# Performance work log

Hardware: AMD Instinct MI355X
Metric: run time of the kernel (lower is better)

The kernel has to match this reference:

```python
import jax, jax.numpy as jnp
import numpy as np

HEAD_SIZE = 256
HEAD_SIZE_R = HEAD_SIZE // 4   # 64, RoPE slice
HEAD_SIZE_C = HEAD_SIZE - HEAD_SIZE_R  # 192
N_EMBD = 256


def rope(x, start_pos=0):
    # x: [B, T, d_r] with interleaved (even, odd) pairs
    B, T, d = x.shape
    half = d // 2
    theta = 1.0 / (10000.0 ** (jnp.arange(half, dtype=x.dtype) / half))  # [half]
    idx = jnp.arange(start_pos, start_pos + T, dtype=x.dtype)[:, None] * theta[None, :]  # [T, half]
    sin, cos = jnp.sin(idx), jnp.cos(idx)
    xs = x.reshape(B, T, half, 2)
    x1, x2 = xs[..., 0], xs[..., 1]
    rot = jnp.stack([x1 * cos - x2 * sin, x1 * sin + x2 * cos], axis=-1)
    return rot.reshape(B, T, d)


def setup_inputs() -> dict:
    key = jax.random.key(0)
    ks = jax.random.split(key, 8)
    B, T = 32, 2048
    s = 0.05
    return {
        "x": jax.random.normal(ks[0], (B, T, N_EMBD), dtype=jnp.float32),
        "Wq_comp": jax.random.normal(ks[1], (N_EMBD, N_EMBD), dtype=jnp.float32) * s,
        "Wkv_comp": jax.random.normal(ks[2], (N_EMBD, N_EMBD), dtype=jnp.float32) * s,
        "Wqc": jax.random.normal(ks[3], (N_EMBD, HEAD_SIZE_C), dtype=jnp.float32) * s,
        "Wqr": jax.random.normal(ks[4], (N_EMBD, HEAD_SIZE_R), dtype=jnp.float32) * s,
        "Wkc": jax.random.normal(ks[5], (N_EMBD, HEAD_SIZE_C), dtype=jnp.float32) * s,
        "Wkr": jax.random.normal(ks[6], (N_EMBD, HEAD_SIZE_R), dtype=jnp.float32) * s,
        "Wv": jax.random.normal(ks[7], (N_EMBD, HEAD_SIZE), dtype=jnp.float32) * s,
    }


def reference(x, Wq_comp, Wkv_comp, Wqc, Wqr, Wkc, Wkr, Wv):
    # Low-rank compression
    c_q = x @ Wq_comp      # [B,T,C]
    c_kv = x @ Wkv_comp    # [B,T,C]
    # Q: content + rotary slice
    q_c = c_q @ Wqc                      # [B,T,192]
    q_r = rope(c_q @ Wqr, start_pos=0)   # [B,T,64]
    q = jnp.concatenate([q_c, q_r], axis=-1)  # [B,T,256]
    # K: content + rotary slice
    k_c = c_kv @ Wkc
    k_r = rope(c_kv @ Wkr, start_pos=0)
    k = jnp.concatenate([k_c, k_r], axis=-1)  # [B,T,256]
    v = c_kv @ Wv                              # [B,T,256]
    # Causal attention (dropout is identity in eval)
    scale = 1.0 / jnp.sqrt(jnp.asarray(HEAD_SIZE, dtype=x.dtype))
    wei = jnp.einsum('bqd,bkd->bqk', q, k) * scale  # [B,T,T]
    T_q = q.shape[1]
    mask = jnp.tril(jnp.ones((T_q, T_q), dtype=bool))
    wei = jnp.where(mask, wei, jnp.asarray(-jnp.inf, dtype=wei.dtype))
    wei = jax.nn.softmax(wei, axis=-1)
    out = jnp.einsum('bqk,bkd->bqd', wei, v)  # [B,T,256]
    return out, (k, v)
```

## Files before the change

### kernel.cpp

```cpp
#include <hip/hip_runtime.h>

typedef float  f32x4  __attribute__((ext_vector_type(4)));
typedef __bf16 bf16x8 __attribute__((ext_vector_type(8)));
typedef unsigned short u16x8 __attribute__((ext_vector_type(8)));
typedef unsigned short u16x4 __attribute__((ext_vector_type(4)));

#define DEV static __device__ __forceinline__

DEV unsigned short f2b(float f) {
  unsigned int u = __float_as_uint(f);
  u += 0x7fffu + ((u >> 16) & 1u);
  return (unsigned short)(u >> 16);
}
DEV float b2f(unsigned short h) { return __uint_as_float(((unsigned int)h) << 16); }

DEV f32x4 mfma16(bf16x8 a, bf16x8 b, f32x4 c) {
  return __builtin_amdgcn_mfma_f32_16x16x32_bf16(a, b, c, 0, 0, 0);
}

__global__ __launch_bounds__(256) void k_prep(
    const float* __restrict__ Wq_comp, const float* __restrict__ Wkv_comp,
    const float* __restrict__ Wqc, const float* __restrict__ Wqr,
    const float* __restrict__ Wkc, const float* __restrict__ Wkr,
    const float* __restrict__ Wv,
    unsigned short* __restrict__ W1t, unsigned short* __restrict__ Wqt,
    unsigned short* __restrict__ Wkvt, float* __restrict__ ct, float* __restrict__ st) {
  int tid = blockIdx.x * 256 + threadIdx.x;
  if (tid < 131072) {
    int n = tid >> 8, k = tid & 255;
    float v = (n < 256) ? Wq_comp[k * 256 + n] : Wkv_comp[k * 256 + (n - 256)];
    W1t[tid] = f2b(v);
  } else if (tid < 196608) {
    int t2 = tid - 131072; int n = t2 >> 8, k = t2 & 255;
    float v = (n < 192) ? Wqc[k * 192 + n] : Wqr[k * 64 + (n - 192)];
    Wqt[t2] = f2b(v);
  } else if (tid < 327680) {
    int t2 = tid - 196608; int n = t2 >> 8, k = t2 & 255;
    float v = (n < 192) ? Wkc[k * 192 + n]
             : (n < 256) ? Wkr[k * 64 + (n - 192)] : Wv[k * 256 + (n - 256)];
    Wkvt[t2] = f2b(v);
  } else if (tid < 393216) {
    int t2 = tid - 327680; int t = t2 >> 5, i = t2 & 31;
    float theta = powf(10000.0f, -(float)i / 32.0f);
    float ang = (float)t * theta;
    ct[t2] = cosf(ang); st[t2] = sinf(ang);
  }
}

__global__ __launch_bounds__(512, 2) void k_gemm1(const float* __restrict__ X,
    const unsigned short* __restrict__ Bt, unsigned short* __restrict__ Cq,
    unsigned short* __restrict__ Ckv) {
  __shared__ __align__(16) unsigned short Ash[128 * 72];
  __shared__ __align__(16) unsigned short Bsh[256 * 72];
  const int nt2 = blockIdx.x, mt = blockIdx.y;
  const int tid = threadIdx.x;
  const int l = tid & 63, wv = tid >> 6, li = l & 15, g = l >> 4;
  const int wm = wv >> 2, wn = wv & 3;
  const f32x4 zf = {0.f, 0.f, 0.f, 0.f};
  f32x4 acc[4][4];
#pragma unroll
  for (int i = 0; i < 4; ++i)
#pragma unroll
    for (int j = 0; j < 4; ++j) acc[i][j] = zf;
  for (int kb = 0; kb < 256; kb += 64) {
    __syncthreads();
#pragma unroll
    for (int it = 0; it < 4; ++it) {
      int idx = it * 512 + tid;
      int row = idx >> 4, c4 = (idx & 15) << 2;
      f32x4 v = *reinterpret_cast<const f32x4*>(X + (size_t)(mt * 128 + row) * 256 + kb + c4);
      u16x4 u = { f2b(v.x), f2b(v.y), f2b(v.z), f2b(v.w) };
      *reinterpret_cast<u16x4*>(&Ash[row * 72 + c4]) = u;
    }
#pragma unroll
    for (int it = 0; it < 4; ++it) {
      int idx = it * 512 + tid;
      int row = idx >> 3, c8 = (idx & 7) << 3;
      *reinterpret_cast<u16x8*>(&Bsh[row * 72 + c8]) =
        *reinterpret_cast<const u16x8*>(Bt + (size_t)(nt2 * 256 + row) * 256 + kb + c8);
    }
    __syncthreads();
#pragma unroll
    for (int kc = 0; kc < 2; ++kc) {
      bf16x8 a[4], b[4];
#pragma unroll
      for (int mf = 0; mf < 4; ++mf)
        a[mf] = *reinterpret_cast<const bf16x8*>(&Ash[(wm * 64 + mf * 16 + li) * 72 + kc * 32 + g * 8]);
#pragma unroll
      for (int nf = 0; nf < 4; ++nf)
        b[nf] = *reinterpret_cast<const bf16x8*>(&Bsh[(wn * 64 + nf * 16 + li) * 72 + kc * 32 + g * 8]);
#pragma unroll
      for (int mf = 0; mf < 4; ++mf)
#pragma unroll
        for (int nf = 0; nf < 4; ++nf)
          acc[mf][nf] = mfma16(a[mf], b[nf], acc[mf][nf]);
    }
  }
  unsigned short* C = nt2 ? Ckv : Cq;
#pragma unroll
  for (int mf = 0; mf < 4; ++mf)
#pragma unroll
    for (int nf = 0; nf < 4; ++nf)
#pragma unroll
      for (int r = 0; r < 4; ++r) {
        int row = mt * 128 + wm * 64 + mf * 16 + g * 4 + r;
        int col = wn * 64 + nf * 16 + li;
        C[(size_t)row * 256 + col] = f2b(acc[mf][nf][r]);
      }
}

__global__ __launch_bounds__(512, 2) void k_gemm2(const unsigned short* __restrict__ Cq,
    const unsigned short* __restrict__ Ckv,
    const unsigned short* __restrict__ Wqt, const unsigned short* __restrict__ Wkvt,
    unsigned short* __restrict__ q_ws, unsigned short* __restrict__ k_ws,
    float* __restrict__ kout, float* __restrict__ vout,
    unsigned short* __restrict__ vt,
    const float* __restrict__ ct, const float* __restrict__ st, int sel0) {
  __shared__ __align__(16) unsigned short Ash[128 * 72];
  __shared__ __align__(16) unsigned short Bsh[256 * 72];
  const int sel = sel0 + blockIdx.x, mt = blockIdx.y;
  const int tid = threadIdx.x;
  const int l = tid & 63, wv = tid >> 6, li = l & 15, g = l >> 4;
  const int wm = wv >> 2, wn = wv & 3;
  const unsigned short* Asrc = (sel == 0) ? Cq : Ckv;
  const unsigned short* Wt = (sel == 0) ? Wqt : Wkvt;
  const int wrow = (sel == 2) ? 256 : 0;
  const f32x4 zf = {0.f, 0.f, 0.f, 0.f};
  f32x4 acc[4][4];
#pragma unroll
  for (int i = 0; i < 4; ++i)
#pragma unroll
    for (int j = 0; j < 4; ++j) acc[i][j] = zf;
  for (int kb = 0; kb < 256; kb += 64) {
    __syncthreads();
#pragma unroll
    for (int it = 0; it < 2; ++it) {
      int idx = it * 512 + tid;
      int row = idx >> 3, c8 = (idx & 7) << 3;
      *reinterpret_cast<u16x8*>(&Ash[row * 72 + c8]) =
        *reinterpret_cast<const u16x8*>(Asrc + (size_t)(mt * 128 + row) * 256 + kb + c8);
    }
#pragma unroll
    for (int it = 0; it < 4; ++it) {
      int idx = it * 512 + tid;
      int row = idx >> 3, c8 = (idx & 7) << 3;
      *reinterpret_cast<u16x8*>(&Bsh[row * 72 + c8]) =
        *reinterpret_cast<const u16x8*>(Wt + (size_t)(wrow + row) * 256 + kb + c8);
    }
    __syncthreads();
#pragma unroll
    for (int kc = 0; kc < 2; ++kc) {
      bf16x8 a[4], b[4];
#pragma unroll
      for (int mf = 0; mf < 4; ++mf)
        a[mf] = *reinterpret_cast<const bf16x8*>(&Ash[(wm * 64 + mf * 16 + li) * 72 + kc * 32 + g * 8]);
#pragma unroll
      for (int nf = 0; nf < 4; ++nf)
        b[nf] = *reinterpret_cast<const bf16x8*>(&Bsh[(wn * 64 + nf * 16 + li) * 72 + kc * 32 + g * 8]);
#pragma unroll
      for (int mf = 0; mf < 4; ++mf)
#pragma unroll
        for (int nf = 0; nf < 4; ++nf)
          acc[mf][nf] = mfma16(a[mf], b[nf], acc[mf][nf]);
    }
  }
  if (sel < 2 && wn == 3) {
#pragma unroll
    for (int mf = 0; mf < 4; ++mf)
#pragma unroll
      for (int nf = 0; nf < 4; ++nf)
#pragma unroll
        for (int r = 0; r < 4; ++r) {
          float v = acc[mf][nf][r];
          float other = __shfl_xor(v, 1);
          int t = (mt * 128 + wm * 64 + mf * 16 + g * 4 + r) & 2047;
          int i = nf * 8 + (li >> 1);
          float c = ct[t * 32 + i], s = st[t * 32 + i];
          acc[mf][nf][r] = (li & 1) ? (other * s + v * c) : (v * c - other * s);
        }
  }
#pragma unroll
  for (int mf = 0; mf < 4; ++mf)
#pragma unroll
    for (int nf = 0; nf < 4; ++nf) {
      int cl = wn * 64 + nf * 16 + li;
#pragma unroll
      for (int r = 0; r < 4; ++r) {
        int row = mt * 128 + wm * 64 + mf * 16 + g * 4 + r;
        float val = acc[mf][nf][r];
        if (sel == 0) {
          q_ws[(size_t)row * 256 + cl] = f2b(val);
        } else if (sel == 1) {
          k_ws[(size_t)row * 256 + cl] = f2b(val);
          kout[(size_t)row * 256 + cl] = val;
        } else {
          vout[(size_t)row * 256 + cl] = val;
        }
      }
    }
  if (sel == 2) {
    const int batch = mt >> 4, tbase = (mt & 15) * 128;
#pragma unroll
    for (int h = 0; h < 2; ++h) {
      __syncthreads();
      if (wm == h) {
#pragma unroll
        for (int mf = 0; mf < 4; ++mf)
#pragma unroll
          for (int nf = 0; nf < 4; ++nf)
#pragma unroll
            for (int r = 0; r < 4; ++r) {
              int lr = mf * 16 + g * 4 + r;
              int col = wn * 64 + nf * 16 + li;
              Bsh[lr * 258 + col] = f2b(acc[mf][nf][r]);
            }
      }
      __syncthreads();
#pragma unroll
      for (int it2 = 0; it2 < 8; ++it2) {
        int idx = it2 * 512 + tid;
        int d = idx >> 4, tq = (idx & 15) << 2;
        u16x4 pk = { Bsh[(tq + 0) * 258 + d], Bsh[(tq + 1) * 258 + d],
                     Bsh[(tq + 2) * 258 + d], Bsh[(tq + 3) * 258 + d] };
        *reinterpret_cast<u16x4*>(vt + ((size_t)batch * 256 + d) * 2048 + tbase + h * 64 + tq) = pk;
      }
    }
  }
}

__global__ __launch_bounds__(512, 2) void k_attn(
    const unsigned short* __restrict__ q_ws, const unsigned short* __restrict__ k_ws,
    const unsigned short* __restrict__ vt_ws, float* __restrict__ out) {
  __shared__ __align__(16) unsigned short Ksh[64 * 256];
  __shared__ __align__(16) unsigned short Vsh[256 * 64];
  __shared__ __align__(16) unsigned short Psh[8][1024];
  const int b = blockIdx.x;
  const int p = blockIdx.y;
  const int tid = threadIdx.x;
  const int l = tid & 63, wv = tid >> 6, li = l & 15, g = l >> 4;
  const f32x4 zf = {0.f, 0.f, 0.f, 0.f};

  u16x8 ones_u = {0x3F80, 0x3F80, 0x3F80, 0x3F80, 0x3F80, 0x3F80, 0x3F80, 0x3F80};
  bf16x8 ones = *reinterpret_cast<bf16x8*>(&ones_u);

  const int s_kr = tid >> 5, s_kc = tid & 31;
  const int s_kpc = s_kc ^ (s_kr & 7);
  const int s_vd = tid >> 3, s_vc = tid & 7;
  const int s_vpc = s_vc ^ (s_vd & 7);

  const unsigned short* kbase = k_ws + (size_t)b * 2048 * 256;
  const unsigned short* vbase = vt_ws + (size_t)b * 256 * 2048;

  u16x8 kreg[4], vreg[4];

  for (int seg = 0; seg < 2; ++seg) {
    const int qt = seg ? (15 - p) : p;
    const int wq0 = qt * 128 + wv * 16;
    bf16x8 qf[8];
    const unsigned short* qp = q_ws + ((size_t)b * 2048 + wq0 + li) * 256;
#pragma unroll
    for (int kc = 0; kc < 8; ++kc)
      qf[kc] = *reinterpret_cast<const bf16x8*>(qp + kc * 32 + g * 8);

    f32x4 o[16];
#pragma unroll
    for (int i = 0; i < 16; ++i) o[i] = zf;
    f32x4 ol = zf;

    const int nj = 2 * qt + 2;
#pragma unroll
    for (int it = 0; it < 4; ++it)
      kreg[it] = *reinterpret_cast<const u16x8*>(kbase + (size_t)(s_kr + it * 16) * 256 + s_kc * 8);
#pragma unroll
    for (int it = 0; it < 4; ++it)
      vreg[it] = *reinterpret_cast<const u16x8*>(vbase + (size_t)(s_vd + it * 64) * 2048 + s_vc * 8);

    for (int j = 0; j < nj; ++j) {
      __syncthreads();
#pragma unroll
      for (int it = 0; it < 4; ++it)
        *reinterpret_cast<u16x8*>(&Ksh[(s_kr + it * 16) * 256 + s_kpc * 8]) = kreg[it];
#pragma unroll
      for (int it = 0; it < 4; ++it)
        *reinterpret_cast<u16x8*>(&Vsh[(s_vd + it * 64) * 64 + s_vpc * 8]) = vreg[it];
      __syncthreads();
      if (j + 1 < nj) {
        const unsigned short* kb2 = kbase + (size_t)(j + 1) * 64 * 256;
        const unsigned short* vb2 = vbase + (size_t)(j + 1) * 64;
#pragma unroll
        for (int it = 0; it < 4; ++it)
          kreg[it] = *reinterpret_cast<const u16x8*>(kb2 + (size_t)(s_kr + it * 16) * 256 + s_kc * 8);
#pragma unroll
        for (int it = 0; it < 4; ++it)
          vreg[it] = *reinterpret_cast<const u16x8*>(vb2 + (size_t)(s_vd + it * 64) * 2048 + s_vc * 8);
      }
      if (j * 64 > qt * 128 + wv * 16 + 15) continue;

      f32x4 s[4];
#pragma unroll
      for (int nf = 0; nf < 4; ++nf) s[nf] = zf;
#pragma unroll
      for (int kc = 0; kc < 8; ++kc) {
        int pc = (kc * 4 + g) ^ (li & 7);
#pragma unroll
        for (int nf = 0; nf < 4; ++nf) {
          bf16x8 bk = *reinterpret_cast<const bf16x8*>(&Ksh[(nf * 16 + li) * 256 + pc * 8]);
          s[nf] = mfma16(qf[kc], bk, s[nf]);
        }
      }
#pragma unroll
      for (int r = 0; r < 4; ++r) {
        const int q = g * 4 + r;
        const int qg = wv * 16 + q;
#pragma unroll
        for (int nf = 0; nf < 4; ++nf) {
          int kg = j * 64 + nf * 16 + li - qt * 128;
          float pv = __expf(__builtin_fmaf(s[nf][r], 0.0625f, -8.0f));
          if (kg > qg) pv = 0.f;
          int kk = nf * 16 + li;
          int pcp = (kk >> 3) ^ (q & 7);
          Psh[wv][q * 64 + pcp * 8 + (kk & 7)] = f2b(pv);
        }
      }
#pragma unroll
      for (int kc2 = 0; kc2 < 2; ++kc2) {
        int pcp = (kc2 * 4 + g) ^ (li & 7);
        bf16x8 pa = *reinterpret_cast<const bf16x8*>(&Psh[wv][li * 64 + pcp * 8]);
        ol = mfma16(pa, ones, ol);
#pragma unroll
        for (int nfd = 0; nfd < 16; ++nfd) {
          bf16x8 bv = *reinterpret_cast<const bf16x8*>(&Vsh[(nfd * 16 + li) * 64 + pcp * 8]);
          o[nfd] = mfma16(pa, bv, o[nfd]);
        }
      }
    }

#pragma unroll
    for (int r = 0; r < 4; ++r) {
      float inv = 1.0f / ol[r];
      int qrow = wq0 + g * 4 + r;
      float* op = out + ((size_t)b * 2048 + qrow) * 256;
#pragma unroll
      for (int nfd = 0; nfd < 16; ++nfd)
        op[nfd * 16 + li] = o[nfd][r] * inv;
    }
  }
}

extern "C" void kernel_launch(void* const* d_in, const int* in_sizes, int n_in,
                              void* d_out, int out_size, void* d_ws, size_t ws_size,
                              hipStream_t stream) {
  const float* x        = (const float*)d_in[0];
  const float* Wq_comp  = (const float*)d_in[1];
  const float* Wkv_comp = (const float*)d_in[2];
  const float* Wqc      = (const float*)d_in[3];
  const float* Wqr      = (const float*)d_in[4];
  const float* Wkc      = (const float*)d_in[5];
  const float* Wkr      = (const float*)d_in[6];
  const float* Wv       = (const float*)d_in[7];

  float* out  = (float*)d_out;
  float* kout = out + 16777216;
  float* vout = out + 33554432;

  if (ws_size < 135397376u) return;

  char* ws = (char*)d_ws;
  unsigned short* c_q  = (unsigned short*)(ws);
  unsigned short* vt   = (unsigned short*)(ws);
  unsigned short* c_kv = (unsigned short*)(ws + 33554432);
  unsigned short* q_ws = (unsigned short*)(ws + 67108864);
  unsigned short* k_ws = (unsigned short*)(ws + 100663296);
  unsigned short* W1t  = (unsigned short*)(ws + 134217728);
  unsigned short* Wqt  = W1t + 131072;
  unsigned short* Wkvt = Wqt + 65536;
  float* ct = (float*)(Wkvt + 131072);
  float* st = ct + 65536;

  k_prep<<<1536, 256, 0, stream>>>(Wq_comp, Wkv_comp, Wqc, Wqr, Wkc, Wkr, Wv,
                                   W1t, Wqt, Wkvt, ct, st);
  k_gemm1<<<dim3(2, 512), 512, 0, stream>>>(x, W1t, c_q, c_kv);
  k_gemm2<<<dim3(2, 512), 512, 0, stream>>>(c_q, c_kv, Wqt, Wkvt, q_ws, k_ws,
                                            kout, vout, vt, ct, st, 0);
  k_gemm2<<<dim3(1, 512), 512, 0, stream>>>(c_q, c_kv, Wqt, Wkvt, q_ws, k_ws,
                                            kout, vout, vt, ct, st, 2);
  k_attn<<<dim3(32, 8), 512, 0, stream>>>(q_ws, k_ws, vt, out);
}
```

Baseline: 263.5 us.

## Pair waves to share P tiles and split PV output across head dimension

Waves are grouped in pairs. Each wave still computes QK^T and the softmax for its own 16 query rows, but the PV product now covers both waves' 32 rows over half of the 256-wide value dimension, reading the partner's P tile from shared memory. Each V fragment loaded from LDS now feeds two MFMAs, which cuts LDS read traffic for V. The cost is an extra workgroup barrier per key tile and an activity check widened to 32 rows, so some waves compute fully masked score tiles.

```diff
diff --git a/kernel.cpp b/kernel.cpp
--- a/kernel.cpp
+++ b/kernel.cpp
@@ -238,6 +238,7 @@
   const int p = blockIdx.y;
   const int tid = threadIdx.x;
   const int l = tid & 63, wv = tid >> 6, li = l & 15, g = l >> 4;
+  const int wp = wv >> 1, wd = wv & 1;
   const f32x4 zf = {0.f, 0.f, 0.f, 0.f};
 
   u16x8 ones_u = {0x3F80, 0x3F80, 0x3F80, 0x3F80, 0x3F80, 0x3F80, 0x3F80, 0x3F80};
@@ -255,17 +256,20 @@
 
   for (int seg = 0; seg < 2; ++seg) {
     const int qt = seg ? (15 - p) : p;
-    const int wq0 = qt * 128 + wv * 16;
+    const int rowbase = qt * 128 + wp * 32;
+    const int own0 = rowbase + wd * 16;
     bf16x8 qf[8];
-    const unsigned short* qp = q_ws + ((size_t)b * 2048 + wq0 + li) * 256;
+    const unsigned short* qp = q_ws + ((size_t)b * 2048 + own0 + li) * 256;
 #pragma unroll
     for (int kc = 0; kc < 8; ++kc)
       qf[kc] = *reinterpret_cast<const bf16x8*>(qp + kc * 32 + g * 8);
 
-    f32x4 o[16];
-#pragma unroll
-    for (int i = 0; i < 16; ++i) o[i] = zf;
-    f32x4 ol = zf;
+    f32x4 o[2][8];
+#pragma unroll
+    for (int i = 0; i < 2; ++i)
+#pragma unroll
+      for (int j2 = 0; j2 < 8; ++j2) o[i][j2] = zf;
+    f32x4 ol[2] = {zf, zf};
 
     const int nj = 2 * qt + 2;
 #pragma unroll
@@ -294,56 +298,69 @@
         for (int it = 0; it < 4; ++it)
           vreg[it] = *reinterpret_cast<const u16x8*>(vb2 + (size_t)(s_vd + it * 64) * 2048 + s_vc * 8);
       }
-      if (j * 64 > qt * 128 + wv * 16 + 15) continue;
-
-      f32x4 s[4];
-#pragma unroll
-      for (int nf = 0; nf < 4; ++nf) s[nf] = zf;
-#pragma unroll
-      for (int kc = 0; kc < 8; ++kc) {
-        int pc = (kc * 4 + g) ^ (li & 7);
-#pragma unroll
-        for (int nf = 0; nf < 4; ++nf) {
-          bf16x8 bk = *reinterpret_cast<const bf16x8*>(&Ksh[(nf * 16 + li) * 256 + pc * 8]);
-          s[nf] = mfma16(qf[kc], bk, s[nf]);
+      const bool active = (j * 64 <= rowbase + 31);
+
+      if (active) {
+        f32x4 s[4];
+#pragma unroll
+        for (int nf = 0; nf < 4; ++nf) s[nf] = zf;
+#pragma unroll
+        for (int kc = 0; kc < 8; ++kc) {
+          int pc = (kc * 4 + g) ^ (li & 7);
+#pragma unroll
+          for (int nf = 0; nf < 4; ++nf) {
+            bf16x8 bk = *reinterpret_cast<const bf16x8*>(&Ksh[(nf * 16 + li) * 256 + pc * 8]);
+            s[nf] = mfma16(qf[kc], bk, s[nf]);
+          }
         }
-      }
+#pragma unroll
+        for (int r = 0; r < 4; ++r) {
+          const int q = g * 4 + r;
+          const int qg = wp * 32 + wd * 16 + q;
+#pragma unroll
+          for (int nf = 0; nf < 4; ++nf) {
+            int kg = j * 64 + nf * 16 + li - qt * 128;
+            float pv = __expf(__builtin_fmaf(s[nf][r], 0.0625f, -8.0f));
+            if (kg > qg) pv = 0.f;
+            int kk = nf * 16 + li;
+            int pcp = (kk >> 3) ^ (q & 7);
+            Psh[wv][q * 64 + pcp * 8 + (kk & 7)] = f2b(pv);
+          }
+        }
+      }
+      asm volatile("s_waitcnt lgkmcnt(0)\n\ts_barrier" ::: "memory");
+      __builtin_amdgcn_sched_barrier(0);
+
+      if (active) {
+#pragma unroll
+        for (int kc2 = 0; kc2 < 2; ++kc2) {
+          int pcp = (kc2 * 4 + g) ^ (li & 7);
+          bf16x8 pa0 = *reinterpret_cast<const bf16x8*>(&Psh[wp * 2 + 0][li * 64 + pcp * 8]);
+          bf16x8 pa1 = *reinterpret_cast<const bf16x8*>(&Psh[wp * 2 + 1][li * 64 + pcp * 8]);
+          ol[0] = mfma16(pa0, ones, ol[0]);
+          ol[1] = mfma16(pa1, ones, ol[1]);
+#pragma unroll
+          for (int nfd = 0; nfd < 8; ++nfd) {
+            int d = wd * 128 + nfd * 16 + li;
+            bf16x8 bv = *reinterpret_cast<const bf16x8*>(&Vsh[d * 64 + pcp * 8]);
+            o[0][nfd] = mfma16(pa0, bv, o[0][nfd]);
+            o[1][nfd] = mfma16(pa1, bv, o[1][nfd]);
+          }
+        }
+      }
+    }
+
+#pragma unroll
+    for (int mf = 0; mf < 2; ++mf)
 #pragma unroll
       for (int r = 0; r < 4; ++r) {
-        const int q = g * 4 + r;
-        const int qg = wv * 16 + q;
-#pragma unroll
-        for (int nf = 0; nf < 4; ++nf) {
-          int kg = j * 64 + nf * 16 + li - qt * 128;
-          float pv = __expf(__builtin_fmaf(s[nf][r], 0.0625f, -8.0f));
-          if (kg > qg) pv = 0.f;
-          int kk = nf * 16 + li;
-          int pcp = (kk >> 3) ^ (q & 7);
-          Psh[wv][q * 64 + pcp * 8 + (kk & 7)] = f2b(pv);
-        }
-      }
-#pragma unroll
-      for (int kc2 = 0; kc2 < 2; ++kc2) {
-        int pcp = (kc2 * 4 + g) ^ (li & 7);
-        bf16x8 pa = *reinterpret_cast<const bf16x8*>(&Psh[wv][li * 64 + pcp * 8]);
-        ol = mfma16(pa, ones, ol);
-#pragma unroll
-        for (int nfd = 0; nfd < 16; ++nfd) {
-          bf16x8 bv = *reinterpret_cast<const bf16x8*>(&Vsh[(nfd * 16 + li) * 64 + pcp * 8]);
-          o[nfd] = mfma16(pa, bv, o[nfd]);
-        }
-      }
-    }
-
-#pragma unroll
-    for (int r = 0; r < 4; ++r) {
-      float inv = 1.0f / ol[r];
-      int qrow = wq0 + g * 4 + r;
-      float* op = out + ((size_t)b * 2048 + qrow) * 256;
-#pragma unroll
-      for (int nfd = 0; nfd < 16; ++nfd)
-        op[nfd * 16 + li] = o[nfd][r] * inv;
-    }
+        float inv = 1.0f / ol[mf][r];
+        int qrow = rowbase + mf * 16 + g * 4 + r;
+        float* op = out + ((size_t)b * 2048 + qrow) * 256 + wd * 128;
+#pragma unroll
+        for (int nfd = 0; nfd < 8; ++nfd)
+          op[nfd * 16 + li] = o[mf][nfd][r] * inv;
+      }
   }
 }
 
```

Result: faster. 257.3 us, median of 2 (-2.4%).
